# Kernel tuning notes

Hardware: AMD Instinct MI355X
Metric: run time of the kernel (lower is better)

## Reference

```python
import math
import jax, jax.numpy as jnp
import numpy as np

N_HEAD = 12

def _alibi_slopes(n):
    def p2(m):
        start = 2 ** (-2 ** (-(math.log2(m) - 3)))
        return [start * start ** i for i in range(m)]
    if math.log2(n).is_integer():
        return p2(n)
    closest = 2 ** math.floor(math.log2(n))
    return p2(closest) + _alibi_slopes(2 * closest)[0::2][: n - closest]


def setup_inputs() -> dict:
    key = jax.random.key(0)
    k1, k2, k3 = jax.random.split(key, 3)
    B, T, C = 2, 2048, 768
    x = jax.random.normal(k1, (B, T, C), dtype=jnp.float32)
    Wqkv = jax.random.normal(k2, (C, 3 * C), dtype=jnp.float32) * 0.02
    bqkv = jnp.zeros((3 * C,), dtype=jnp.float32)
    Wproj = jax.random.normal(k3, (C, C), dtype=jnp.float32) * 0.02
    bproj = jnp.zeros((C,), dtype=jnp.float32)
    return {"x": x, "Wqkv": Wqkv, "bqkv": bqkv, "Wproj": Wproj, "bproj": bproj}


def reference(x, Wqkv, bqkv, Wproj, bproj):
    B, T, C = x.shape
    H = N_HEAD
    D = C // H

    qkv = x @ Wqkv + bqkv                       # (B, T, 3C)
    q, k, v = jnp.split(qkv, 3, axis=-1)
    q = q.reshape(B, T, H, D).transpose(0, 2, 1, 3)  # (B, H, T, D)
    k = k.reshape(B, T, H, D).transpose(0, 2, 1, 3)
    v = v.reshape(B, T, H, D).transpose(0, 2, 1, 3)

    scores = jnp.einsum('bhqd,bhkd->bhqk', q, k) / math.sqrt(D)  # (B,H,T,T)

    # ALiBi: subtract slope * clamp(j - i, 0)
    slopes = jnp.asarray(_alibi_slopes(H), dtype=scores.dtype).reshape(1, H, 1, 1)
    pos = jnp.arange(T)
    rel = jnp.clip(pos[None, :] - pos[:, None], 0)               # (T, T) int
    scores = scores - slopes * rel.astype(scores.dtype)[None, None]

    # causal mask: j > i -> -inf
    causal = pos[None, :] > pos[:, None]
    scores = jnp.where(causal[None, None], -jnp.inf, scores)

    att = jax.nn.softmax(scores, axis=-1)                        # (B,H,T,T)
    y = jnp.einsum('bhqk,bhkd->bhqd', att, v)                    # (B,H,T,D)
    y = y.transpose(0, 2, 1, 3).reshape(B, T, C)
    y = y @ Wproj + bproj
    return (y, att)
```

## Files before the change

### kernel.cpp

```cpp
#include <hip/hip_runtime.h>
#include <math.h>


#define LOG2E 1.4426950408889634f

typedef __attribute__((ext_vector_type(8))) short bf16x8;
typedef __attribute__((ext_vector_type(4))) float f32x4;

__device__ __forceinline__ unsigned short f2bf(float f) {
  unsigned int u = __builtin_bit_cast(unsigned int, f);
  u = (u + 0x7fffu + ((u >> 16) & 1u)) >> 16;
  return (unsigned short)u;
}

__global__ void k_convert(const float* __restrict__ in, unsigned short* __restrict__ out, int n4) {
  int i = blockIdx.x * blockDim.x + threadIdx.x;
  int stride = gridDim.x * blockDim.x;
  for (; i < n4; i += stride) {
    float4 v = reinterpret_cast<const float4*>(in)[i];
    ushort4 o;
    o.x = f2bf(v.x); o.y = f2bf(v.y); o.z = f2bf(v.z); o.w = f2bf(v.w);
    reinterpret_cast<ushort4*>(out)[i] = o;
  }
}

__global__ void k_transpose(const float* __restrict__ in, unsigned short* __restrict__ out, int K, int N) {
  int idx = blockIdx.x * blockDim.x + threadIdx.x;
  if (idx >= K * N) return;
  int k = idx / N, n = idx - k * N;
  out[(size_t)n * K + k] = f2bf(in[idx]);
}

__global__ __launch_bounds__(256) void k_gemm(
    const unsigned short* __restrict__ A,
    const unsigned short* __restrict__ Bt,
    const float* __restrict__ bias,
    int M, int N, int K, int mode,
    unsigned short* __restrict__ qb,
    unsigned short* __restrict__ kb,
    unsigned short* __restrict__ vb,
    float* __restrict__ yout)
{
  __shared__ __align__(16) unsigned short As[128 * 64];
  __shared__ __align__(16) unsigned short Bs[128 * 64];
  const int bm = blockIdx.x, bn = blockIdx.y;
  const int tid = threadIdx.x;
  const int lane = tid & 63, wid = tid >> 6;
  const int wr = wid >> 1, wc = wid & 1;
  const int lr = lane & 15, lg = lane >> 4;

  f32x4 acc[4][4] = {};

  for (int k0 = 0; k0 < K; k0 += 64) {
    __syncthreads();
#pragma unroll
    for (int i = 0; i < 4; ++i) {
      int c = tid + i * 256;
      int row = c >> 3, g = c & 7;
      int sw = ((g ^ (row & 7)) * 8);
      *reinterpret_cast<bf16x8*>(&As[row * 64 + sw]) =
          *reinterpret_cast<const bf16x8*>(&A[(size_t)(bm * 128 + row) * K + k0 + g * 8]);
      *reinterpret_cast<bf16x8*>(&Bs[row * 64 + sw]) =
          *reinterpret_cast<const bf16x8*>(&Bt[(size_t)(bn * 128 + row) * K + k0 + g * 8]);
    }
    __syncthreads();
#pragma unroll
    for (int kk = 0; kk < 2; ++kk) {
      const int g = kk * 4 + lg;
      bf16x8 af[4], bfrag[4];
#pragma unroll
      for (int f = 0; f < 4; ++f) {
        int ra = wr * 64 + f * 16 + lr;
        af[f] = *reinterpret_cast<const bf16x8*>(&As[ra * 64 + ((g ^ (ra & 7)) * 8)]);
        int rb = wc * 64 + f * 16 + lr;
        bfrag[f] = *reinterpret_cast<const bf16x8*>(&Bs[rb * 64 + ((g ^ (rb & 7)) * 8)]);
      }
#pragma unroll
      for (int fm = 0; fm < 4; ++fm)
#pragma unroll
        for (int fn = 0; fn < 4; ++fn)
          acc[fm][fn] = __builtin_amdgcn_mfma_f32_16x16x32_bf16(af[fm], bfrag[fn], acc[fm][fn], 0, 0, 0);
    }
  }

#pragma unroll
  for (int fm = 0; fm < 4; ++fm)
#pragma unroll
    for (int fn = 0; fn < 4; ++fn) {
      int col = bn * 128 + wc * 64 + fn * 16 + lr;
      float bi = bias[col];
#pragma unroll
      for (int r = 0; r < 4; ++r) {
        int rowm = bm * 128 + wr * 64 + fm * 16 + lg * 4 + r;
        float val = acc[fm][fn][r] + bi;
        if (mode == 0) {
          int which = col / 768;
          int c = col - which * 768;
          int h = c >> 6, d = c & 63;
          int b = rowm >> 11, t = rowm & 2047;
          size_t bh = (size_t)b * 12 + h;
          unsigned short uv = f2bf(val);
          if (which == 0)      qb[(bh * 2048 + t) * 64 + d] = uv;
          else if (which == 1) kb[(bh * 2048 + t) * 64 + d] = uv;
          else                 vb[(bh * 64 + d) * 2048 + t] = uv;
        } else {
          yout[(size_t)rowm * N + col] = val;
        }
      }
    }
}

__global__ __launch_bounds__(256) void k_attn(
    const unsigned short* __restrict__ qb,
    const unsigned short* __restrict__ kb,
    const unsigned short* __restrict__ vb,
    float* __restrict__ att,
    unsigned short* __restrict__ yh)
{
  __shared__ __align__(16) unsigned short Ks[64 * 64];
  __shared__ __align__(16) unsigned short Vs[64 * 64];
  __shared__ __align__(16) unsigned short Ps[4][16 * 64];

  const int qt = blockIdx.x;
  const int bh = blockIdx.y;
  const int tid = threadIdx.x;
  const int lane = tid & 63, wid = tid >> 6;
  const int lr = lane & 15, lg = lane >> 4;

  const unsigned short* Qg = qb + ((size_t)bh * 2048 + qt * 64) * 64;
  const unsigned short* Kg = kb + (size_t)bh * 2048 * 64;
  const unsigned short* Vg = vb + (size_t)bh * 64 * 2048;
  float* attg = att + ((size_t)bh * 2048 + qt * 64) * 2048;

  bf16x8 qf[2];
#pragma unroll
  for (int kk = 0; kk < 2; ++kk)
    qf[kk] = *reinterpret_cast<const bf16x8*>(&Qg[(wid * 16 + lr) * 64 + kk * 32 + lg * 8]);

  const int qrow_l = wid * 16 + lg * 4;

  float m_r[4], l_r[4];
#pragma unroll
  for (int r = 0; r < 4; ++r) { m_r[r] = -__builtin_inff(); l_r[r] = 0.f; }

  for (int kt = 0; kt <= qt; ++kt) {
    __syncthreads();
#pragma unroll
    for (int i = 0; i < 2; ++i) {
      int c = tid + i * 256;
      int row = c >> 3, g = c & 7;
      *reinterpret_cast<bf16x8*>(&Ks[row * 64 + ((g ^ (row & 7)) * 8)]) =
          *reinterpret_cast<const bf16x8*>(&Kg[(kt * 64 + row) * 64 + g * 8]);
    }
    __syncthreads();

    f32x4 s[4] = {};
#pragma unroll
    for (int kk = 0; kk < 2; ++kk) {
      int g = kk * 4 + lg;
#pragma unroll
      for (int fc = 0; fc < 4; ++fc) {
        int row = fc * 16 + lr;
        bf16x8 kf = *reinterpret_cast<const bf16x8*>(&Ks[row * 64 + ((g ^ (row & 7)) * 8)]);
        s[fc] = __builtin_amdgcn_mfma_f32_16x16x32_bf16(qf[kk], kf, s[fc], 0, 0, 0);
      }
    }

#pragma unroll
    for (int r = 0; r < 4; ++r) {
      float sv[4];
      float mx = -__builtin_inff();
#pragma unroll
      for (int fc = 0; fc < 4; ++fc) {
        float x = s[fc][r] * 0.125f;
        if (kt == qt && (fc * 16 + lr) > (qrow_l + r)) x = -__builtin_inff();
        sv[fc] = x;
        mx = fmaxf(mx, x);
      }
#pragma unroll
      for (int d = 1; d < 16; d <<= 1) mx = fmaxf(mx, __shfl_xor(mx, d));
      float mnew = fmaxf(m_r[r], mx);
      float sum = 0.f;
#pragma unroll
      for (int fc = 0; fc < 4; ++fc) sum += exp2f((sv[fc] - mnew) * LOG2E);
#pragma unroll
      for (int d = 1; d < 16; d <<= 1) sum += __shfl_xor(sum, d);
      l_r[r] = l_r[r] * exp2f((m_r[r] - mnew) * LOG2E) + sum;
      m_r[r] = mnew;
    }
  }

  float rcp_l[4];
#pragma unroll
  for (int r = 0; r < 4; ++r) rcp_l[r] = 1.0f / l_r[r];

  f32x4 o[4] = {};
  for (int kt = 0; kt <= qt; ++kt) {
    __syncthreads();
#pragma unroll
    for (int i = 0; i < 2; ++i) {
      int c = tid + i * 256;
      int row = c >> 3, g = c & 7;
      *reinterpret_cast<bf16x8*>(&Ks[row * 64 + ((g ^ (row & 7)) * 8)]) =
          *reinterpret_cast<const bf16x8*>(&Kg[(kt * 64 + row) * 64 + g * 8]);
      *reinterpret_cast<bf16x8*>(&Vs[row * 64 + ((g ^ (row & 7)) * 8)]) =
          *reinterpret_cast<const bf16x8*>(&Vg[(size_t)row * 2048 + kt * 64 + g * 8]);
    }
    __syncthreads();

    f32x4 s[4] = {};
#pragma unroll
    for (int kk = 0; kk < 2; ++kk) {
      int g = kk * 4 + lg;
#pragma unroll
      for (int fc = 0; fc < 4; ++fc) {
        int row = fc * 16 + lr;
        bf16x8 kf = *reinterpret_cast<const bf16x8*>(&Ks[row * 64 + ((g ^ (row & 7)) * 8)]);
        s[fc] = __builtin_amdgcn_mfma_f32_16x16x32_bf16(qf[kk], kf, s[fc], 0, 0, 0);
      }
    }

#pragma unroll
    for (int fc = 0; fc < 4; ++fc)
#pragma unroll
      for (int r = 0; r < 4; ++r) {
        float x = s[fc][r] * 0.125f;
        bool masked = (kt == qt) && ((fc * 16 + lr) > (qrow_l + r));
        float p = masked ? 0.f : exp2f((x - m_r[r]) * LOG2E);
        attg[(size_t)(qrow_l + r) * 2048 + kt * 64 + fc * 16 + lr] = p * rcp_l[r];
        int pr = lg * 4 + r;
        int col = fc * 16 + lr;
        Ps[wid][pr * 64 + (((col >> 3) ^ (pr & 7)) * 8) + (col & 7)] = f2bf(p);
      }

    __syncthreads();

#pragma unroll
    for (int kk = 0; kk < 2; ++kk) {
      int g = kk * 4 + lg;
      bf16x8 pa = *reinterpret_cast<const bf16x8*>(&Ps[wid][lr * 64 + ((g ^ (lr & 7)) * 8)]);
#pragma unroll
      for (int fc = 0; fc < 4; ++fc) {
        int row = fc * 16 + lr;
        bf16x8 vf = *reinterpret_cast<const bf16x8*>(&Vs[row * 64 + ((g ^ (row & 7)) * 8)]);
        o[fc] = __builtin_amdgcn_mfma_f32_16x16x32_bf16(pa, vf, o[fc], 0, 0, 0);
      }
    }
  }

  {
    int W = 2048 - (qt + 1) * 64;
    if (W > 0) {
      int base = (qt + 1) * 64;
      int Wq = W >> 2;
      int n4 = 64 * Wq;
      float4 z = {0.f, 0.f, 0.f, 0.f};
      for (int i = tid; i < n4; i += 256) {
        int row = i / Wq, c4 = i - row * Wq;
        *reinterpret_cast<float4*>(&attg[(size_t)row * 2048 + base + c4 * 4]) = z;
      }
    }
  }

  {
    int b = bh / 12, h = bh - b * 12;
#pragma unroll
    for (int fc = 0; fc < 4; ++fc)
#pragma unroll
      for (int r = 0; r < 4; ++r) {
        int tg = qt * 64 + qrow_l + r;
        yh[((size_t)b * 2048 + tg) * 768 + h * 64 + fc * 16 + lr] = f2bf(o[fc][r] * rcp_l[r]);
      }
  }
}

extern "C" void kernel_launch(void* const* d_in, const int* in_sizes, int n_in,
                              void* d_out, int out_size, void* d_ws, size_t ws_size,
                              hipStream_t stream) {
  const float* x     = (const float*)d_in[0];
  const float* Wqkv  = (const float*)d_in[1];
  const float* bqkv  = (const float*)d_in[2];
  const float* Wproj = (const float*)d_in[3];
  const float* bproj = (const float*)d_in[4];

  float* y   = (float*)d_out;
  float* att = y + (size_t)2 * 2048 * 768;

  char* ws = (char*)d_ws;
  unsigned short* xb     = (unsigned short*)(ws);
  unsigned short* wqkvT  = (unsigned short*)(ws + 6291456);
  unsigned short* wprojT = (unsigned short*)(ws + 9830400);
  unsigned short* qb     = (unsigned short*)(ws + 11010048);
  unsigned short* kb     = (unsigned short*)(ws + 17301504);
  unsigned short* vb     = (unsigned short*)(ws + 23592960);
  unsigned short* yh     = (unsigned short*)(ws + 29884416);

  k_convert<<<1024, 256, 0, stream>>>(x, xb, (2 * 2048 * 768) / 4);
  k_transpose<<<(768 * 2304 + 255) / 256, 256, 0, stream>>>(Wqkv, wqkvT, 768, 2304);
  k_transpose<<<(768 * 768 + 255) / 256, 256, 0, stream>>>(Wproj, wprojT, 768, 768);

  k_gemm<<<dim3(32, 18), 256, 0, stream>>>(xb, wqkvT, bqkv, 4096, 2304, 768, 0,
                                           qb, kb, vb, nullptr);
  k_attn<<<dim3(32, 24), 256, 0, stream>>>(qb, kb, vb, att, yh);
  k_gemm<<<dim3(32, 6), 256, 0, stream>>>(yh, wprojT, bproj, 4096, 768, 768, 1,
                                          nullptr, nullptr, nullptr, y);
}
```

Before: 639.7 us.

## Coalesce V stores via separate transpose, tile weight transposes, reverse attention tile order

```diff
diff --git a/kernel.cpp b/kernel.cpp
--- a/kernel.cpp
+++ b/kernel.cpp
@@ -24,11 +24,34 @@
   }
 }
 
-__global__ void k_transpose(const float* __restrict__ in, unsigned short* __restrict__ out, int K, int N) {
-  int idx = blockIdx.x * blockDim.x + threadIdx.x;
-  if (idx >= K * N) return;
-  int k = idx / N, n = idx - k * N;
-  out[(size_t)n * K + k] = f2bf(in[idx]);
+__global__ __launch_bounds__(256) void k_transpose_w(const float* __restrict__ in,
+                                                     unsigned short* __restrict__ out,
+                                                     int K, int N) {
+  __shared__ float tile[32][33];
+  const int bk = blockIdx.x * 32, bn = blockIdx.y * 32;
+  const int tr = threadIdx.x >> 5, tc = threadIdx.x & 31;
+#pragma unroll
+  for (int i = 0; i < 4; ++i)
+    tile[tr + i * 8][tc] = in[(size_t)(bk + tr + i * 8) * N + bn + tc];
+  __syncthreads();
+#pragma unroll
+  for (int i = 0; i < 4; ++i)
+    out[(size_t)(bn + tr + i * 8) * K + bk + tc] = f2bf(tile[tc][tr + i * 8]);
+}
+
+__global__ __launch_bounds__(256) void k_transpose_v(const unsigned short* __restrict__ in,
+                                                     unsigned short* __restrict__ out) {
+  __shared__ unsigned short tile[32][34];
+  const int bt = blockIdx.x * 32, bd = blockIdx.y * 32;
+  const size_t base = (size_t)blockIdx.z * 2048 * 64;
+  const int tr = threadIdx.x >> 5, tc = threadIdx.x & 31;
+#pragma unroll
+  for (int i = 0; i < 4; ++i)
+    tile[tr + i * 8][tc] = in[base + (size_t)(bt + tr + i * 8) * 64 + bd + tc];
+  __syncthreads();
+#pragma unroll
+  for (int i = 0; i < 4; ++i)
+    out[base + (size_t)(bd + tr + i * 8) * 2048 + bt + tc] = tile[tc][tr + i * 8];
 }
 
 __global__ __launch_bounds__(256) void k_gemm(
@@ -100,9 +123,10 @@
           int b = rowm >> 11, t = rowm & 2047;
           size_t bh = (size_t)b * 12 + h;
           unsigned short uv = f2bf(val);
-          if (which == 0)      qb[(bh * 2048 + t) * 64 + d] = uv;
-          else if (which == 1) kb[(bh * 2048 + t) * 64 + d] = uv;
-          else                 vb[(bh * 64 + d) * 2048 + t] = uv;
+          size_t idx = (bh * 2048 + t) * 64 + d;
+          if (which == 0)      qb[idx] = uv;
+          else if (which == 1) kb[idx] = uv;
+          else                 vb[idx] = uv;
         } else {
           yout[(size_t)rowm * N + col] = val;
         }
@@ -113,7 +137,7 @@
 __global__ __launch_bounds__(256) void k_attn(
     const unsigned short* __restrict__ qb,
     const unsigned short* __restrict__ kb,
-    const unsigned short* __restrict__ vb,
+    const unsigned short* __restrict__ vT,
     float* __restrict__ att,
     unsigned short* __restrict__ yh)
 {
@@ -121,7 +145,7 @@
   __shared__ __align__(16) unsigned short Vs[64 * 64];
   __shared__ __align__(16) unsigned short Ps[4][16 * 64];
 
-  const int qt = blockIdx.x;
+  const int qt = gridDim.x - 1 - blockIdx.x;
   const int bh = blockIdx.y;
   const int tid = threadIdx.x;
   const int lane = tid & 63, wid = tid >> 6;
@@ -129,7 +153,7 @@
 
   const unsigned short* Qg = qb + ((size_t)bh * 2048 + qt * 64) * 64;
   const unsigned short* Kg = kb + (size_t)bh * 2048 * 64;
-  const unsigned short* Vg = vb + (size_t)bh * 64 * 2048;
+  const unsigned short* Vg = vT + (size_t)bh * 64 * 2048;
   float* attg = att + ((size_t)bh * 2048 + qt * 64) * 2048;
 
   bf16x8 qf[2];
@@ -232,8 +256,6 @@
         int col = fc * 16 + lr;
         Ps[wid][pr * 64 + (((col >> 3) ^ (pr & 7)) * 8) + (col & 7)] = f2bf(p);
       }
-
-    __syncthreads();
 
 #pragma unroll
     for (int kk = 0; kk < 2; ++kk) {
@@ -294,14 +316,16 @@
   unsigned short* kb     = (unsigned short*)(ws + 17301504);
   unsigned short* vb     = (unsigned short*)(ws + 23592960);
   unsigned short* yh     = (unsigned short*)(ws + 29884416);
+  unsigned short* vT     = xb;
 
   k_convert<<<1024, 256, 0, stream>>>(x, xb, (2 * 2048 * 768) / 4);
-  k_transpose<<<(768 * 2304 + 255) / 256, 256, 0, stream>>>(Wqkv, wqkvT, 768, 2304);
-  k_transpose<<<(768 * 768 + 255) / 256, 256, 0, stream>>>(Wproj, wprojT, 768, 768);
+  k_transpose_w<<<dim3(24, 72), 256, 0, stream>>>(Wqkv, wqkvT, 768, 2304);
+  k_transpose_w<<<dim3(24, 24), 256, 0, stream>>>(Wproj, wprojT, 768, 768);
 
   k_gemm<<<dim3(32, 18), 256, 0, stream>>>(xb, wqkvT, bqkv, 4096, 2304, 768, 0,
                                            qb, kb, vb, nullptr);
-  k_attn<<<dim3(32, 24), 256, 0, stream>>>(qb, kb, vb, att, yh);
+  k_transpose_v<<<dim3(64, 2, 24), 256, 0, stream>>>(vb, vT);
+  k_attn<<<dim3(32, 24), 256, 0, stream>>>(qb, kb, vT, att, yh);
   k_gemm<<<dim3(32, 6), 256, 0, stream>>>(yh, wprojT, bproj, 4096, 768, 768, 1,
                                           nullptr, nullptr, nullptr, y);
 }
```

Measured after the change: 647.3 us. About the same (+1.2%).
